# Optimization experiments

Measured on AMD Instinct MI355X. Metric: run time of the kernel, lower is better.

## Reference

```python
import jax, jax.numpy as jnp
import numpy as np

G, N, K, H, D = 16, 256, 128, 32, 768
NUM_ATOM_TYPES = 128
NUM_EDGE_TYPES = NUM_ATOM_TYPES * NUM_ATOM_TYPES  # 16384
T_STEPS = 1000


def setup_inputs() -> dict:
    key = jax.random.key(0)
    ks = jax.random.split(key, 12)
    return {
        "pos": jax.random.normal(ks[0], (G, N, 3), dtype=jnp.float32) * 3.0,
        "x": jax.random.randint(ks[1], (G, N, 1), 0, NUM_ATOM_TYPES, dtype=jnp.int32),
        "t": jax.random.randint(ks[2], (G,), 0, T_STEPS, dtype=jnp.int32),
        "means": jax.random.uniform(ks[3], (T_STEPS, K), jnp.float32, 0.0, 3.0),
        "stds": jax.random.uniform(ks[4], (T_STEPS, K), jnp.float32, 0.0, 3.0),
        "mul_w": jnp.ones((NUM_EDGE_TYPES, 1), jnp.float32),
        "bias_w": jnp.zeros((NUM_EDGE_TYPES, 1), jnp.float32),
        "w1": jax.random.normal(ks[5], (K, K), jnp.float32) / np.sqrt(K),
        "b1": jnp.zeros((K,), jnp.float32),
        "w2": jax.random.normal(ks[6], (K, H), jnp.float32) / np.sqrt(K),
        "b2": jnp.zeros((H,), jnp.float32),
        "we": jax.random.normal(ks[7], (K, D), jnp.float32) / np.sqrt(K),
        "be": jnp.zeros((D,), jnp.float32),
    }


def _forward(pos, x, t, means, stds, mul_w, bias_w, w1, b1, w2, b2, we, be):
    atoms = x[:, :, 0]  # [G, N]
    edge_types = atoms[:, :, None] * NUM_ATOM_TYPES + atoms[:, None, :]  # [G,N,N]
    pad = atoms == 0  # [G, N]
    pos = jnp.where(pad[..., None], 0.0, pos)
    # delta_pos[g,i,j] = pos[g,j] - pos[g,i]
    delta_pos = pos[:, None, :, :] - pos[:, :, None, :]  # [G,N,N,3]
    sq = jnp.sum(delta_pos * delta_pos, axis=-1)  # [G,N,N]
    dist = jnp.sqrt(jnp.where(sq > 0, sq, 1.0)) * (sq > 0)  # safe norm, grad-safe at 0
    delta_pos = delta_pos / (dist[..., None] + 1e-5)
    # Gaussian basis expansion
    mul = mul_w[edge_types]   # [G,N,N,1]
    bias = bias_w[edge_types]  # [G,N,N,1]
    xg = mul * dist[..., None] + bias  # [G,N,N,1] -> broadcasts to K
    mean = means[t][:, None, None, :]               # [G,1,1,K]
    std = jnp.abs(stds[t])[:, None, None, :] + 1e-5  # [G,1,1,K]
    a = (2.0 * 3.14159) ** 0.5
    z = (xg - mean) / std
    edge_feature = jnp.exp(-0.5 * z * z) / (a * std)  # [G,N,N,K]
    # NonLinear MLP -> attn bias per head
    h = jax.nn.gelu(edge_feature @ w1 + b1, approximate=False)
    attn_bias = h @ w2 + b2  # [G,N,N,H]
    attn_bias = jnp.transpose(attn_bias, (0, 3, 1, 2))  # [G,H,N,N]
    attn_bias = jnp.where(pad[:, None, None, :], -jnp.inf, attn_bias)
    # masked sum over source nodes + edge projection
    ef = jnp.where(pad[:, None, :, None], 0.0, edge_feature)
    sum_ef = jnp.sum(ef, axis=-2)  # [G,N,K]
    merge = sum_ef @ we + be  # [G,N,D]
    return dist, delta_pos, attn_bias, merge


def reference(pos, x, t, means, stds, mul_w, bias_w, w1, b1, w2, b2, we, be):
    return _forward(pos, x, t, means, stds, mul_w, bias_w, w1, b1, w2, b2, we, be)
```

## Files before the change

### kernel.cpp

```cpp
#include <hip/hip_runtime.h>
#include <hip/hip_bf16.h>
#include <math.h>

#define Gn 16
#define Nn 256
#define Kf 128
#define Hh 32
#define Dd 768
#define NEG_BIG (-3.0e38f)
#define PAD_XG  (1.0e10f)
#define INV_A 0.3989422804014327f
#define NHALF_LOG2E (-0.7213475204444817f)
#define GELU_C (-2.4554669f)

typedef __attribute__((ext_vector_type(8))) short bf16x8;
typedef __attribute__((ext_vector_type(4))) float f32x4;
typedef __attribute__((ext_vector_type(2))) float f32x2;

static __device__ __forceinline__ float fast_exp2(float x) {
#if __has_builtin(__builtin_amdgcn_exp2f)
    return __builtin_amdgcn_exp2f(x);
#else
    return exp2f(x);
#endif
}
static __device__ __forceinline__ float fast_rcp(float x) {
#if __has_builtin(__builtin_amdgcn_rcpf)
    return __builtin_amdgcn_rcpf(x);
#else
    return 1.0f / x;
#endif
}

static __device__ __forceinline__ unsigned short f2bf(float f) {
    union { float f; unsigned int u; } v; v.f = f;
    unsigned int r = v.u + 0x7FFF + ((v.u >> 16) & 1);
    return (unsigned short)(r >> 16);
}

static __device__ __forceinline__ void load_lds16(const void* g, void* l) {
    __builtin_amdgcn_global_load_lds(
        (const __attribute__((address_space(1))) unsigned int*)g,
        (__attribute__((address_space(3))) unsigned int*)l, 16, 0, 0);
}

static __device__ __forceinline__ void stage8k(const char* gsrc, char* lbase,
                                               int wq, int lane) {
    const char* g0 = gsrc + wq * 1024 + lane * 16;
    char* l0 = lbase + wq * 1024 + lane * 16;
    load_lds16(g0, l0);
    load_lds16(g0 + 4096, l0 + 4096);
}

__global__ __launch_bounds__(256)
void prep_kernel(const float* __restrict__ w1, const float* __restrict__ w2,
                 const int* __restrict__ tarr, const float* __restrict__ means,
                 const float* __restrict__ stds,
                 char* __restrict__ w1c, char* __restrict__ w2s,
                 float4* __restrict__ coef)
{
    const int idx = blockIdx.x * 256 + threadIdx.x;
    if (idx < 2048) {
        const int ks = idx >> 9;
        const int n  = (idx >> 2) & 127;
        const int s  = idx & 3;
        unsigned short v[8];
#pragma unroll
        for (int e = 0; e < 8; ++e) {
            const int k = ks * 32 + s * 8 + e;
            v[e] = f2bf(w1[k * Kf + n]);
        }
        *(uint4*)(w1c + ks * 8192 + n * 64 + ((s ^ (n & 3)) << 4)) =
            *(const uint4*)v;
    } else if (idx < 2560) {
        const int e2 = idx - 2048;
        const int m = e2 >> 4, s2 = e2 & 15;
        unsigned short v[8];
#pragma unroll
        for (int e = 0; e < 8; ++e) {
            const int k = s2 * 8 + e;
            v[e] = f2bf(w2[k * Hh + m]);
        }
        *(uint4*)(w2s + m * 256 + ((s2 ^ (m & 7)) << 4)) = *(const uint4*)v;
    } else if (idx < 4608) {
        const int e3 = idx - 2560;
        const int g = e3 >> 7, k = e3 & 127;
        const int tg = tarr[g];
        const float mean = means[tg * Kf + k];
        const float sd   = fabsf(stds[tg * Kf + k]) + 1e-5f;
        const float inv  = 1.0f / sd;
        coef[g * Kf + k] =
            make_float4(mean, NHALF_LOG2E * inv * inv, log2f(inv * INV_A), 0.f);
    }
}

__global__ __launch_bounds__(256, 4)
void graph3d_attn_kernel(const float* __restrict__ pos,
                         const int* __restrict__ atoms,
                         const float* __restrict__ mul_w,
                         const float* __restrict__ bias_w,
                         const float* __restrict__ b1,
                         const float* __restrict__ b2,
                         const char* __restrict__ w1c,
                         const char* __restrict__ w2s,
                         const float4* __restrict__ coef,
                         float* __restrict__ ws_sum,
                         float* __restrict__ out_dist,
                         float* __restrict__ out_delta,
                         float* __restrict__ out_attn)
{
    const int tid  = threadIdx.x;
    const int half = blockIdx.x;
    const int i    = blockIdx.y;
    const int g    = blockIdx.z;
    const int j0   = half * 128;

    __shared__ __align__(16) unsigned short s_tile[128 * 128];
    __shared__ __align__(16) unsigned short s_chunk[4096];

    const int lane = tid & 63, wq = tid >> 6;
    const int l15 = lane & 15, lhi = lane >> 4;

    if (tid < 128) {
        const int ai = atoms[g * Nn + i];
        float pix = pos[(g * Nn + i) * 3 + 0];
        float piy = pos[(g * Nn + i) * 3 + 1];
        float piz = pos[(g * Nn + i) * 3 + 2];
        if (ai == 0) { pix = 0.f; piy = 0.f; piz = 0.f; }

        const int j  = j0 + tid;
        const int aj = atoms[g * Nn + j];
        float pjx = pos[(g * Nn + j) * 3 + 0];
        float pjy = pos[(g * Nn + j) * 3 + 1];
        float pjz = pos[(g * Nn + j) * 3 + 2];
        if (aj == 0) { pjx = 0.f; pjy = 0.f; pjz = 0.f; }
        const float dx = pjx - pix, dy = pjy - piy, dz = pjz - piz;
        const float sq = dx * dx + dy * dy + dz * dz;
        const float dist = (sq > 0.f) ? sqrtf(sq) : 0.f;
        const float inv_d = 1.f / (dist + 1e-5f);
        const size_t base = (size_t)(g * Nn + i) * Nn + j;
        out_dist[base] = dist;
        out_delta[base * 3 + 0] = dx * inv_d;
        out_delta[base * 3 + 1] = dy * inv_d;
        out_delta[base * 3 + 2] = dz * inv_d;
        const int et = ai * 128 + aj;
        float xg = fmaf(mul_w[et], dist, bias_w[et]);
        if (aj == 0) xg = PAD_XG;
        *(float*)((char*)s_tile + (size_t)((tid >> 5) * 32 + 31) * 256 +
                  (tid & 31) * 4) = xg;
    }
    __syncthreads();

    stage8k(w1c, (char*)s_chunk, wq, lane);

    f32x2 ps = (f32x2){0.f, 0.f};
    {
        const float4 c0 = coef[g * Kf + 2 * lane];
        const float4 c1 = coef[g * Kf + 2 * lane + 1];
        const f32x2 mn = (f32x2){c0.x, c1.x};
        const f32x2 Ak = (f32x2){c0.y, c1.y};
        const f32x2 Ck = (f32x2){c0.z, c1.z};
        char* rowbase = (char*)s_tile + wq * 32 * 256;
        const float* xgp = (const float*)((char*)s_tile + (wq * 32 + 31) * 256);
        const int colb = 4 * lane;
#pragma unroll 8
        for (int jj = 0; jj < 32; ++jj) {
            const float xgj = xgp[jj];
            f32x2 d = (f32x2){xgj, xgj} - mn;
            f32x2 t = Ak * (d * d) + Ck;
            const float e0 = fast_exp2(t.x);
            const float e1 = fast_exp2(t.y);
            ps += (f32x2){e0, e1};
            const __hip_bfloat162 p = __float22bfloat162_rn(make_float2(e0, e1));
            *(unsigned int*)(rowbase + jj * 256 + (colb ^ ((jj & 7) << 4))) =
                *(const unsigned int*)&p;
        }
    }
    __syncthreads();

    const int jrow0 = wq * 32 + l15, jrow1 = jrow0 + 16;
    const char* tb0 = (const char*)s_tile + jrow0 * 256;
    const char* tb1 = (const char*)s_tile + jrow1 * 256;
    const int sw0 = (jrow0 & 7) << 4, sw1 = (jrow1 & 7) << 4;
    const int aoff = l15 * 64 + ((lhi ^ (l15 & 3)) << 4);

    f32x4 acc[8][2];
#pragma unroll
    for (int a = 0; a < 8; ++a)
#pragma unroll
        for (int b = 0; b < 2; ++b) acc[a][b] = (f32x4){0.f, 0.f, 0.f, 0.f};

#pragma unroll
    for (int ks = 0; ks < 4; ++ks) {
        if (ks) __syncthreads();
        const int kb = ks * 64 + lhi * 16;
        const bf16x8 b0  = *(const bf16x8*)(tb0 + (kb ^ sw0));
        const bf16x8 b1f = *(const bf16x8*)(tb1 + (kb ^ sw1));
        bf16x8 a0[4];
#pragma unroll
        for (int nf = 0; nf < 4; ++nf)
            a0[nf] = *(const bf16x8*)((const char*)s_chunk + nf * 1024 + aoff);
#pragma unroll
        for (int nf = 0; nf < 4; ++nf) {
            acc[nf][0] = __builtin_amdgcn_mfma_f32_16x16x32_bf16(a0[nf], b0,  acc[nf][0], 0, 0, 0);
            acc[nf][1] = __builtin_amdgcn_mfma_f32_16x16x32_bf16(a0[nf], b1f, acc[nf][1], 0, 0, 0);
        }
        bf16x8 a1[4];
#pragma unroll
        for (int nf = 0; nf < 4; ++nf)
            a1[nf] = *(const bf16x8*)((const char*)s_chunk + (nf + 4) * 1024 + aoff);
        __syncthreads();
        if (ks < 3) stage8k(w1c + (ks + 1) * 8192, (char*)s_chunk, wq, lane);
        else        stage8k(w2s, (char*)s_chunk, wq, lane);
#pragma unroll
        for (int nf = 0; nf < 4; ++nf) {
            acc[nf + 4][0] = __builtin_amdgcn_mfma_f32_16x16x32_bf16(a1[nf], b0,  acc[nf + 4][0], 0, 0, 0);
            acc[nf + 4][1] = __builtin_amdgcn_mfma_f32_16x16x32_bf16(a1[nf], b1f, acc[nf + 4][1], 0, 0, 0);
        }
    }

#pragma unroll
    for (int nf = 0; nf < 8; ++nf) {
        const float4 bbv = *(const float4*)(b1 + nf * 16 + lhi * 4);
        const f32x4 bb = (f32x4){bbv.x, bbv.y, bbv.z, bbv.w};
        const int colb = 32 * nf + 8 * lhi;
#pragma unroll
        for (int jf = 0; jf < 2; ++jf) {
            const char* tb = jf ? tb1 : tb0;
            const int sw = jf ? sw1 : sw0;
            const f32x4 v = acc[nf][jf] + bb;
            const f32x4 arg = v * GELU_C;
            f32x4 den;
            den.x = fast_exp2(arg.x); den.y = fast_exp2(arg.y);
            den.z = fast_exp2(arg.z); den.w = fast_exp2(arg.w);
            den += 1.0f;
            f32x4 h;
            h.x = v.x * fast_rcp(den.x); h.y = v.y * fast_rcp(den.y);
            h.z = v.z * fast_rcp(den.z); h.w = v.w * fast_rcp(den.w);
            const __hip_bfloat162 p0 = __float22bfloat162_rn(make_float2(h.x, h.y));
            const __hip_bfloat162 p1 = __float22bfloat162_rn(make_float2(h.z, h.w));
            uint2 u;
            u.x = *(const unsigned int*)&p0;
            u.y = *(const unsigned int*)&p1;
            *(uint2*)(const_cast<char*>(tb) + (colb ^ sw)) = u;
        }
    }
    __syncthreads();

    f32x4 acc2[2][2];
#pragma unroll
    for (int a = 0; a < 2; ++a)
#pragma unroll
        for (int b = 0; b < 2; ++b) acc2[a][b] = (f32x4){0.f, 0.f, 0.f, 0.f};

#pragma unroll
    for (int ks = 0; ks < 4; ++ks) {
        const int kb = ks * 64 + lhi * 16;
        const bf16x8 bh0 = *(const bf16x8*)(tb0 + (kb ^ sw0));
        const bf16x8 bh1 = *(const bf16x8*)(tb1 + (kb ^ sw1));
#pragma unroll
        for (int mf = 0; mf < 2; ++mf) {
            const int m = mf * 16 + l15;
            const bf16x8 a2 = *(const bf16x8*)((const char*)s_chunk + m * 256 + (kb ^ ((m & 7) << 4)));
            acc2[mf][0] = __builtin_amdgcn_mfma_f32_16x16x32_bf16(a2, bh0, acc2[mf][0], 0, 0, 0);
            acc2[mf][1] = __builtin_amdgcn_mfma_f32_16x16x32_bf16(a2, bh1, acc2[mf][1], 0, 0, 0);
        }
    }

    __syncthreads();
    {
        float* pt = (float*)s_tile;
        *(f32x2*)&pt[wq * 128 + 2 * lane] = ps;
    }
    __syncthreads();
    if (tid < 128) {
        const float* pt = (const float*)s_tile;
        const float s = (pt[tid] + pt[128 + tid]) + (pt[256 + tid] + pt[384 + tid]);
        ws_sum[((size_t)(g * Nn + i) * 2 + half) * Kf + tid] = s;
    }

    const size_t attn_g = (size_t)g * Hh * (Nn * Nn) + (size_t)i * Nn + j0;
#pragma unroll
    for (int jf = 0; jf < 2; ++jf) {
        const int jloc = wq * 32 + jf * 16 + l15;
        const bool keep = atoms[g * Nn + j0 + jloc] != 0;
#pragma unroll
        for (int mf = 0; mf < 2; ++mf) {
            const float4 b2v = *(const float4*)(b2 + mf * 16 + lhi * 4);
            const f32x4 bv = (f32x4){b2v.x, b2v.y, b2v.z, b2v.w};
            const f32x4 v = acc2[mf][jf] + bv;
#pragma unroll
            for (int r = 0; r < 4; ++r) {
                const int m = mf * 16 + lhi * 4 + r;
                out_attn[attn_g + (size_t)m * (Nn * Nn) + jloc] =
                    keep ? v[r] : NEG_BIG;
            }
        }
    }
}

__global__ __launch_bounds__(256)
void graph3d_merge_kernel(const float* __restrict__ ws_sum,
                          const float* __restrict__ we,
                          const float* __restrict__ be,
                          float* __restrict__ out_merge)
{
    const int tid = threadIdx.x;
    const int bd  = blockIdx.x;
    const int r0  = blockIdx.y * 16;
    __shared__ __align__(16) float s_rows[16][128];

#pragma unroll
    for (int p = 0; p < 8; ++p) {
        const int e = p * 256 + tid;
        const int r = e >> 7, k = e & 127;
        const size_t gi = (size_t)(r0 + r);
        s_rows[r][k] = ws_sum[(gi * 2 + 0) * Kf + k] + ws_sum[(gi * 2 + 1) * Kf + k];
    }
    __syncthreads();

    const int col = bd * 256 + tid;
    float acc[16];
#pragma unroll
    for (int r = 0; r < 16; ++r) acc[r] = 0.f;

    for (int k4 = 0; k4 < 32; ++k4) {
        const int k = k4 * 4;
        const float w0  = we[(k + 0) * Dd + col];
        const float w1v = we[(k + 1) * Dd + col];
        const float w2v = we[(k + 2) * Dd + col];
        const float w3  = we[(k + 3) * Dd + col];
#pragma unroll
        for (int r = 0; r < 16; ++r) {
            const float4 s = ((const float4*)&s_rows[r][0])[k4];
            acc[r] = fmaf(s.x, w0, acc[r]);
            acc[r] = fmaf(s.y, w1v, acc[r]);
            acc[r] = fmaf(s.z, w2v, acc[r]);
            acc[r] = fmaf(s.w, w3, acc[r]);
        }
    }

    const float b = be[col];
#pragma unroll
    for (int r = 0; r < 16; ++r)
        out_merge[(size_t)(r0 + r) * Dd + col] = acc[r] + b;
}

extern "C" void kernel_launch(void* const* d_in, const int* in_sizes, int n_in,
                              void* d_out, int out_size, void* d_ws, size_t ws_size,
                              hipStream_t stream) {
    const float* pos    = (const float*)d_in[0];
    const int*   x      = (const int*)  d_in[1];
    const int*   t      = (const int*)  d_in[2];
    const float* means  = (const float*)d_in[3];
    const float* stds   = (const float*)d_in[4];
    const float* mul_w  = (const float*)d_in[5];
    const float* bias_w = (const float*)d_in[6];
    const float* w1     = (const float*)d_in[7];
    const float* b1     = (const float*)d_in[8];
    const float* w2     = (const float*)d_in[9];
    const float* b2     = (const float*)d_in[10];
    const float* we     = (const float*)d_in[11];
    const float* be     = (const float*)d_in[12];

    float* out = (float*)d_out;
    float* out_dist  = out;
    float* out_delta = out + (size_t)Gn * Nn * Nn;
    float* out_attn  = out + (size_t)Gn * Nn * Nn * 4;
    float* out_merge = out + (size_t)Gn * Nn * Nn * 4 + (size_t)Gn * Hh * Nn * Nn;

    float* ws_sum = (float*)d_ws;
    char*  w1c  = (char*)d_ws + (size_t)Gn * Nn * 2 * Kf * 4;
    char*  w2s  = w1c + 4 * 8192;
    float4* coef = (float4*)(w2s + 8192);

    prep_kernel<<<18, 256, 0, stream>>>(w1, w2, t, means, stds, w1c, w2s, coef);

    dim3 gridA(2, Nn, Gn);
    graph3d_attn_kernel<<<gridA, 256, 0, stream>>>(
        pos, x, mul_w, bias_w, b1, b2, w1c, w2s, coef,
        ws_sum, out_dist, out_delta, out_attn);

    dim3 gridB(3, 256);
    graph3d_merge_kernel<<<gridB, 256, 0, stream>>>(
        ws_sum, we, be, out_merge);
}
```

Before: 121.3 us.

## Compute Gaussian MFMA fragments in registers and move edge-sum to separate kernel

The Gaussian basis values are no longer written to a shared-memory tile before the first GEMM. Each lane now computes its bf16 B-fragments directly in registers per k-chunk, and the next chunk's fragments are computed while the current MFMAs run. The per-row edge-feature sum moves out of the attention kernel into a new sumef_kernel, which recomputes distances and exponentials. The w1 swizzle also gains an extra XOR term to reduce LDS bank conflicts. This trades redundant exp work (four lanes per row share the same k values, plus the duplicate recompute in the new kernel) for fewer LDS round trips and barriers.

```diff
diff --git a/kernel.cpp b/kernel.cpp
--- a/kernel.cpp
+++ b/kernel.cpp
@@ -15,7 +15,6 @@
 
 typedef __attribute__((ext_vector_type(8))) short bf16x8;
 typedef __attribute__((ext_vector_type(4))) float f32x4;
-typedef __attribute__((ext_vector_type(2))) float f32x2;
 
 static __device__ __forceinline__ float fast_exp2(float x) {
 #if __has_builtin(__builtin_amdgcn_exp2f)
@@ -70,8 +69,8 @@
             const int k = ks * 32 + s * 8 + e;
             v[e] = f2bf(w1[k * Kf + n]);
         }
-        *(uint4*)(w1c + ks * 8192 + n * 64 + ((s ^ (n & 3)) << 4)) =
-            *(const uint4*)v;
+        *(uint4*)(w1c + ks * 8192 + n * 64 +
+                  ((s ^ (n & 3) ^ ((n >> 2) & 3)) << 4)) = *(const uint4*)v;
     } else if (idx < 2560) {
         const int e2 = idx - 2048;
         const int m = e2 >> 4, s2 = e2 & 15;
@@ -94,6 +93,30 @@
     }
 }
 
+static __device__ __forceinline__ void compute_frags(
+    const float4* __restrict__ cbase, int ks, int lhi,
+    float xg0, float xg1, bf16x8* f0, bf16x8* f1)
+{
+    union { bf16x8 v; unsigned int w[4]; } u0, u1;
+    const float4* cp = cbase + ks * 32 + lhi * 8;
+#pragma unroll
+    for (int e2 = 0; e2 < 4; ++e2) {
+        const float4 ca = cp[2 * e2];
+        const float4 cb = cp[2 * e2 + 1];
+        float d, ea, eb;
+        d = xg0 - ca.x; ea = fast_exp2(fmaf(ca.y, d * d, ca.z));
+        d = xg0 - cb.x; eb = fast_exp2(fmaf(cb.y, d * d, cb.z));
+        const __hip_bfloat162 p0 = __float22bfloat162_rn(make_float2(ea, eb));
+        u0.w[e2] = *(const unsigned int*)&p0;
+        d = xg1 - ca.x; ea = fast_exp2(fmaf(ca.y, d * d, ca.z));
+        d = xg1 - cb.x; eb = fast_exp2(fmaf(cb.y, d * d, cb.z));
+        const __hip_bfloat162 p1 = __float22bfloat162_rn(make_float2(ea, eb));
+        u1.w[e2] = *(const unsigned int*)&p1;
+    }
+    *f0 = u0.v;
+    *f1 = u1.v;
+}
+
 __global__ __launch_bounds__(256, 4)
 void graph3d_attn_kernel(const float* __restrict__ pos,
                          const int* __restrict__ atoms,
@@ -104,7 +127,6 @@
                          const char* __restrict__ w1c,
                          const char* __restrict__ w2s,
                          const float4* __restrict__ coef,
-                         float* __restrict__ ws_sum,
                          float* __restrict__ out_dist,
                          float* __restrict__ out_delta,
                          float* __restrict__ out_attn)
@@ -146,43 +168,24 @@
         const int et = ai * 128 + aj;
         float xg = fmaf(mul_w[et], dist, bias_w[et]);
         if (aj == 0) xg = PAD_XG;
-        *(float*)((char*)s_tile + (size_t)((tid >> 5) * 32 + 31) * 256 +
-                  (tid & 31) * 4) = xg;
+        ((float*)s_tile)[tid] = xg;
     }
     __syncthreads();
 
+    const float xg0 = ((float*)s_tile)[wq * 32 + l15];
+    const float xg1 = ((float*)s_tile)[wq * 32 + l15 + 16];
+
     stage8k(w1c, (char*)s_chunk, wq, lane);
 
-    f32x2 ps = (f32x2){0.f, 0.f};
-    {
-        const float4 c0 = coef[g * Kf + 2 * lane];
-        const float4 c1 = coef[g * Kf + 2 * lane + 1];
-        const f32x2 mn = (f32x2){c0.x, c1.x};
-        const f32x2 Ak = (f32x2){c0.y, c1.y};
-        const f32x2 Ck = (f32x2){c0.z, c1.z};
-        char* rowbase = (char*)s_tile + wq * 32 * 256;
-        const float* xgp = (const float*)((char*)s_tile + (wq * 32 + 31) * 256);
-        const int colb = 4 * lane;
-#pragma unroll 8
-        for (int jj = 0; jj < 32; ++jj) {
-            const float xgj = xgp[jj];
-            f32x2 d = (f32x2){xgj, xgj} - mn;
-            f32x2 t = Ak * (d * d) + Ck;
-            const float e0 = fast_exp2(t.x);
-            const float e1 = fast_exp2(t.y);
-            ps += (f32x2){e0, e1};
-            const __hip_bfloat162 p = __float22bfloat162_rn(make_float2(e0, e1));
-            *(unsigned int*)(rowbase + jj * 256 + (colb ^ ((jj & 7) << 4))) =
-                *(const unsigned int*)&p;
-        }
-    }
-    __syncthreads();
+    const float4* cbase = coef + g * Kf;
+    bf16x8 fc0, fc1;
+    compute_frags(cbase, 0, lhi, xg0, xg1, &fc0, &fc1);
 
     const int jrow0 = wq * 32 + l15, jrow1 = jrow0 + 16;
-    const char* tb0 = (const char*)s_tile + jrow0 * 256;
-    const char* tb1 = (const char*)s_tile + jrow1 * 256;
+    char* tb0 = (char*)s_tile + jrow0 * 256;
+    char* tb1 = (char*)s_tile + jrow1 * 256;
     const int sw0 = (jrow0 & 7) << 4, sw1 = (jrow1 & 7) << 4;
-    const int aoff = l15 * 64 + ((lhi ^ (l15 & 3)) << 4);
+    const int aoff = l15 * 64 + ((lhi ^ (l15 & 3) ^ ((l15 >> 2) & 3)) << 4);
 
     f32x4 acc[8][2];
 #pragma unroll
@@ -192,18 +195,15 @@
 
 #pragma unroll
     for (int ks = 0; ks < 4; ++ks) {
-        if (ks) __syncthreads();
-        const int kb = ks * 64 + lhi * 16;
-        const bf16x8 b0  = *(const bf16x8*)(tb0 + (kb ^ sw0));
-        const bf16x8 b1f = *(const bf16x8*)(tb1 + (kb ^ sw1));
+        __syncthreads();
         bf16x8 a0[4];
 #pragma unroll
         for (int nf = 0; nf < 4; ++nf)
             a0[nf] = *(const bf16x8*)((const char*)s_chunk + nf * 1024 + aoff);
 #pragma unroll
         for (int nf = 0; nf < 4; ++nf) {
-            acc[nf][0] = __builtin_amdgcn_mfma_f32_16x16x32_bf16(a0[nf], b0,  acc[nf][0], 0, 0, 0);
-            acc[nf][1] = __builtin_amdgcn_mfma_f32_16x16x32_bf16(a0[nf], b1f, acc[nf][1], 0, 0, 0);
+            acc[nf][0] = __builtin_amdgcn_mfma_f32_16x16x32_bf16(a0[nf], fc0, acc[nf][0], 0, 0, 0);
+            acc[nf][1] = __builtin_amdgcn_mfma_f32_16x16x32_bf16(a0[nf], fc1, acc[nf][1], 0, 0, 0);
         }
         bf16x8 a1[4];
 #pragma unroll
@@ -212,11 +212,15 @@
         __syncthreads();
         if (ks < 3) stage8k(w1c + (ks + 1) * 8192, (char*)s_chunk, wq, lane);
         else        stage8k(w2s, (char*)s_chunk, wq, lane);
+        bf16x8 fn0, fn1;
+        if (ks < 3)
+            compute_frags(cbase, ks + 1, lhi, xg0, xg1, &fn0, &fn1);
 #pragma unroll
         for (int nf = 0; nf < 4; ++nf) {
-            acc[nf + 4][0] = __builtin_amdgcn_mfma_f32_16x16x32_bf16(a1[nf], b0,  acc[nf + 4][0], 0, 0, 0);
-            acc[nf + 4][1] = __builtin_amdgcn_mfma_f32_16x16x32_bf16(a1[nf], b1f, acc[nf + 4][1], 0, 0, 0);
-        }
+            acc[nf + 4][0] = __builtin_amdgcn_mfma_f32_16x16x32_bf16(a1[nf], fc0, acc[nf + 4][0], 0, 0, 0);
+            acc[nf + 4][1] = __builtin_amdgcn_mfma_f32_16x16x32_bf16(a1[nf], fc1, acc[nf + 4][1], 0, 0, 0);
+        }
+        if (ks < 3) { fc0 = fn0; fc1 = fn1; }
     }
 
 #pragma unroll
@@ -226,7 +230,7 @@
         const int colb = 32 * nf + 8 * lhi;
 #pragma unroll
         for (int jf = 0; jf < 2; ++jf) {
-            const char* tb = jf ? tb1 : tb0;
+            char* tb = jf ? tb1 : tb0;
             const int sw = jf ? sw1 : sw0;
             const f32x4 v = acc[nf][jf] + bb;
             const f32x4 arg = v * GELU_C;
@@ -242,7 +246,7 @@
             uint2 u;
             u.x = *(const unsigned int*)&p0;
             u.y = *(const unsigned int*)&p1;
-            *(uint2*)(const_cast<char*>(tb) + (colb ^ sw)) = u;
+            *(uint2*)(tb + (colb ^ sw)) = u;
         }
     }
     __syncthreads();
@@ -267,28 +271,17 @@
         }
     }
 
-    __syncthreads();
-    {
-        float* pt = (float*)s_tile;
-        *(f32x2*)&pt[wq * 128 + 2 * lane] = ps;
-    }
-    __syncthreads();
-    if (tid < 128) {
-        const float* pt = (const float*)s_tile;
-        const float s = (pt[tid] + pt[128 + tid]) + (pt[256 + tid] + pt[384 + tid]);
-        ws_sum[((size_t)(g * Nn + i) * 2 + half) * Kf + tid] = s;
-    }
-
     const size_t attn_g = (size_t)g * Hh * (Nn * Nn) + (size_t)i * Nn + j0;
+    const float4 b2lo = *(const float4*)(b2 + lhi * 4);
+    const float4 b2hi = *(const float4*)(b2 + 16 + lhi * 4);
 #pragma unroll
     for (int jf = 0; jf < 2; ++jf) {
         const int jloc = wq * 32 + jf * 16 + l15;
         const bool keep = atoms[g * Nn + j0 + jloc] != 0;
 #pragma unroll
         for (int mf = 0; mf < 2; ++mf) {
-            const float4 b2v = *(const float4*)(b2 + mf * 16 + lhi * 4);
-            const f32x4 bv = (f32x4){b2v.x, b2v.y, b2v.z, b2v.w};
-            const f32x4 v = acc2[mf][jf] + bv;
+            const float4 b2v = mf ? b2hi : b2lo;
+            const f32x4 v = acc2[mf][jf] + (f32x4){b2v.x, b2v.y, b2v.z, b2v.w};
 #pragma unroll
             for (int r = 0; r < 4; ++r) {
                 const int m = mf * 16 + lhi * 4 + r;
@@ -296,6 +289,75 @@
                     keep ? v[r] : NEG_BIG;
             }
         }
+    }
+}
+
+__global__ __launch_bounds__(256)
+void sumef_kernel(const float* __restrict__ pos,
+                  const int* __restrict__ atoms,
+                  const float* __restrict__ mul_w,
+                  const float* __restrict__ bias_w,
+                  const float4* __restrict__ coef,
+                  float* __restrict__ ws_sum)
+{
+    const int tid = threadIdx.x;
+    const int i0  = blockIdx.x * 4;
+    const int g   = blockIdx.y;
+
+    __shared__ float s_xg[4][Nn];
+    __shared__ float s_part[2][4][Kf];
+
+    {
+        const int j  = tid;
+        const int aj = atoms[g * Nn + j];
+        float pjx = pos[(g * Nn + j) * 3 + 0];
+        float pjy = pos[(g * Nn + j) * 3 + 1];
+        float pjz = pos[(g * Nn + j) * 3 + 2];
+        if (aj == 0) { pjx = 0.f; pjy = 0.f; pjz = 0.f; }
+#pragma unroll
+        for (int ii = 0; ii < 4; ++ii) {
+            const int iv = i0 + ii;
+            const int ai = atoms[g * Nn + iv];
+            float pix = pos[(g * Nn + iv) * 3 + 0];
+            float piy = pos[(g * Nn + iv) * 3 + 1];
+            float piz = pos[(g * Nn + iv) * 3 + 2];
+            if (ai == 0) { pix = 0.f; piy = 0.f; piz = 0.f; }
+            const float dx = pjx - pix, dy = pjy - piy, dz = pjz - piz;
+            const float sq = dx * dx + dy * dy + dz * dz;
+            const float dist = (sq > 0.f) ? sqrtf(sq) : 0.f;
+            const int et = ai * 128 + aj;
+            float xg = fmaf(mul_w[et], dist, bias_w[et]);
+            if (aj == 0) xg = PAD_XG;
+            s_xg[ii][j] = xg;
+        }
+    }
+    __syncthreads();
+
+    {
+        const int k  = tid & 127;
+        const int jh = tid >> 7;
+        const float4 c = coef[g * Kf + k];
+        float p0 = 0.f, p1 = 0.f, p2 = 0.f, p3 = 0.f;
+        const int jb = jh * 128;
+#pragma unroll 4
+        for (int j = jb; j < jb + 128; ++j) {
+            float d;
+            d = s_xg[0][j] - c.x; p0 += fast_exp2(fmaf(c.y, d * d, c.z));
+            d = s_xg[1][j] - c.x; p1 += fast_exp2(fmaf(c.y, d * d, c.z));
+            d = s_xg[2][j] - c.x; p2 += fast_exp2(fmaf(c.y, d * d, c.z));
+            d = s_xg[3][j] - c.x; p3 += fast_exp2(fmaf(c.y, d * d, c.z));
+        }
+        s_part[jh][0][k] = p0; s_part[jh][1][k] = p1;
+        s_part[jh][2][k] = p2; s_part[jh][3][k] = p3;
+    }
+    __syncthreads();
+
+#pragma unroll
+    for (int q = 0; q < 2; ++q) {
+        const int e = q * 256 + tid;
+        const int ii = e >> 7, k = e & 127;
+        ws_sum[(size_t)(g * Nn + i0 + ii) * Kf + k] =
+            s_part[0][ii][k] + s_part[1][ii][k];
     }
 }
 
@@ -314,8 +376,7 @@
     for (int p = 0; p < 8; ++p) {
         const int e = p * 256 + tid;
         const int r = e >> 7, k = e & 127;
-        const size_t gi = (size_t)(r0 + r);
-        s_rows[r][k] = ws_sum[(gi * 2 + 0) * Kf + k] + ws_sum[(gi * 2 + 1) * Kf + k];
+        s_rows[r][k] = ws_sum[(size_t)(r0 + r) * Kf + k];
     }
     __syncthreads();
 
@@ -379,7 +440,10 @@
     dim3 gridA(2, Nn, Gn);
     graph3d_attn_kernel<<<gridA, 256, 0, stream>>>(
         pos, x, mul_w, bias_w, b1, b2, w1c, w2s, coef,
-        ws_sum, out_dist, out_delta, out_attn);
+        out_dist, out_delta, out_attn);
+
+    dim3 gridS(Nn / 4, Gn);
+    sumef_kernel<<<gridS, 256, 0, stream>>>(pos, x, mul_w, bias_w, coef, ws_sum);
 
     dim3 gridB(3, 256);
     graph3d_merge_kernel<<<gridB, 256, 0, stream>>>(
```

Measured after the change: 153.2 us. 26.3% more time.
